# Performance work log

Hardware: AMD Instinct MI355X
Metric: run time of the kernel (lower is better)

## Reference

```python
import jax, jax.numpy as jnp
import numpy as np

EPS = 1e-5
KERNELS = [3, 3, 5, 7]  # 2*i+1 for i>=1, first layer k=3


def _conv_relu_bn(x, w, b, gamma, beta, rmean, rvar):
    # x: [B, Cin, S], w: [Cout, Cin, K]
    k = w.shape[-1]
    y = jax.lax.conv_general_dilated(
        x, w, window_strides=(1,), padding=[(k // 2, k // 2)],
        dimension_numbers=("NCW", "OIW", "NCW"))
    y = y + b[None, :, None]
    y = jax.nn.relu(y)
    # BatchNorm1d in inference mode (running stats)
    inv = gamma[None, :, None] / jnp.sqrt(rvar[None, :, None] + EPS)
    return (y - rmean[None, :, None]) * inv + beta[None, :, None]


def setup_inputs() -> dict:
    key = jax.random.key(0)
    ks = jax.random.split(key, 32)
    B, S = 128, 8192
    inp = {"x": jax.random.normal(ks[0], (B, 4, S), dtype=jnp.float32)}
    cin = 4
    for i, k in enumerate(KERNELS):
        inp[f"w{i}"] = jax.random.normal(ks[1 + i], (32, cin, k), dtype=jnp.float32) * 0.1
        inp[f"b{i}"] = jnp.zeros((32,), jnp.float32)
        inp[f"g{i}"] = jnp.ones((32,), jnp.float32)   # BN gamma
        inp[f"bb{i}"] = jnp.zeros((32,), jnp.float32)  # BN beta
        inp[f"rm{i}"] = jnp.zeros((32,), jnp.float32)  # running mean
        inp[f"rv{i}"] = jnp.ones((32,), jnp.float32)   # running var
        cin = 32
    inp["fw1"] = jax.random.normal(ks[10], (16, 32), dtype=jnp.float32) * 0.1
    inp["fb1"] = jnp.zeros((16,), jnp.float32)
    inp["fw2"] = jax.random.normal(ks[11], (1, 16), dtype=jnp.float32) * 0.1
    inp["fb2"] = jnp.zeros((1,), jnp.float32)
    return inp


def reference(x,
              w0, b0, g0, bb0, rm0, rv0,
              w1, b1, g1, bb1, rm1, rv1,
              w2, b2, g2, bb2, rm2, rv2,
              w3, b3, g3, bb3, rm3, rv3,
              fw1, fb1, fw2, fb2):
    x = _conv_relu_bn(x, w0, b0, g0, bb0, rm0, rv0)
    x = _conv_relu_bn(x, w1, b1, g1, bb1, rm1, rv1)
    x = _conv_relu_bn(x, w2, b2, g2, bb2, rm2, rv2)
    x = _conv_relu_bn(x, w3, b3, g3, bb3, rm3, rv3)
    # [B, 32, S] -> [B, S, 32]; the original per-timestep MLP loop is one batched GEMM
    h = jnp.einsum("bcs,hc->bsh", x, fw1) + fb1
    h = jax.nn.relu(h)  # Dropout(0.1) is identity in eval
    out = jnp.einsum("bsh,oh->bso", h, fw2) + fb2
    return out[..., 0]  # squeeze(-1) -> [B, S]
```

## Files before the change

### kernel.cpp

```cpp
#include <hip/hip_runtime.h>

#define SEQ    8192
#define S_TILE 180
#define NROW   198
#define CS     1608
#define NTHR   256
#define NREC   33
#define BN_HALFOFF (NREC*512)

typedef __attribute__((ext_vector_type(8))) _Float16 half8;
typedef __attribute__((ext_vector_type(4))) float    f32x4;

__device__ __forceinline__ int uni(int v){ return __builtin_amdgcn_readfirstlane(v); }

template<int K>
__device__ __forceinline__ float fold_bias(const float* __restrict__ W, int co,
    const float* __restrict__ gp, const float* __restrict__ bbp,
    const float* __restrict__ rmp, const float* __restrict__ rvp)
{
    float acc = 0.f;
#pragma unroll
    for (int ci = 0; ci < 32; ++ci) {
        float sp = gp[ci] * rsqrtf(rvp[ci] + 1e-5f);
        float tp = bbp[ci] - rmp[ci]*sp;
        float wsum = 0.f;
#pragma unroll
        for (int tap = 0; tap < K; ++tap) wsum += W[(co*32 + ci)*K + tap];
        acc += wsum * tp;
    }
    return acc;
}

extern "C" __global__ void prep_kernel(
    const float* w0, const float* w1, const float* w2, const float* w3,
    const float* b0, const float* g0, const float* bb0, const float* rm0, const float* rv0,
    const float* b1, const float* g1, const float* bb1, const float* rm1, const float* rv1,
    const float* b2, const float* g2, const float* bb2, const float* rm2, const float* rv2,
    const float* b3, const float* g3, const float* bb3, const float* rm3, const float* rv3,
    const float* fw1, const float* fb1, _Float16* ws)
{
    const int tid = threadIdx.x;
    const int rec = blockIdx.x;
    if (rec < NREC) {
        if (tid < 64) {
            const int lane = tid;
            const int q = lane >> 4;
            half8 h;
            if (rec < 2) {
                int co = rec*16 + (lane & 15);
#pragma unroll
                for (int j = 0; j < 8; ++j) {
                    int k = q*8 + j;
                    float wv = (k < 12) ? w0[(co*4 + (k & 3))*3 + (k >> 2)] : 0.0f;
                    h[j] = (_Float16)wv;
                }
            } else {
                const float* W; const float *gp, *rvp; int K, r2;
                if      (rec < 8)  { W = w1;  K = 3; r2 = rec - 2;  gp = g0; rvp = rv0; }
                else if (rec < 18) { W = w2;  K = 5; r2 = rec - 8;  gp = g1; rvp = rv1; }
                else if (rec < 32) { W = w3;  K = 7; r2 = rec - 18; gp = g2; rvp = rv2; }
                else               { W = fw1; K = 1; r2 = 0;        gp = g3; rvp = rv3; }
                int tap = r2 >> 1, mh = r2 & 1;
                int co  = mh*16 + (lane & 15);
#pragma unroll
                for (int j = 0; j < 8; ++j) {
                    int ci = ((j >> 2) << 4) + q*4 + (j & 3);
                    float wv = W[(co*32 + ci)*K + tap];
                    wv *= gp[ci] * rsqrtf(rvp[ci] + 1e-5f);
                    h[j] = (_Float16)wv;
                }
            }
            *(half8*)(ws + rec*512 + lane*8) = h;
        }
    } else {
        float* fa = (float*)(ws + BN_HALFOFF);
        if (tid < 128) {
            int l = tid >> 5, co = tid & 31;
            const float *g, *bb, *rm, *rv, *bi;
            if      (l == 0) { g=g0; bb=bb0; rm=rm0; rv=rv0; bi=b0; }
            else if (l == 1) { g=g1; bb=bb1; rm=rm1; rv=rv1; bi=b1; }
            else if (l == 2) { g=g2; bb=bb2; rm=rm2; rv=rv2; bi=b2; }
            else             { g=g3; bb=bb3; rm=rm3; rv=rv3; bi=b3; }
            float s = g[co] * rsqrtf(rv[co] + 1e-5f);
            float t = bb[co] - rm[co]*s;
            float bias = bi[co];
            if      (l == 1) bias += fold_bias<3>(w1, co, g0, bb0, rm0, rv0);
            else if (l == 2) bias += fold_bias<5>(w2, co, g1, bb1, rm1, rv1);
            else if (l == 3) bias += fold_bias<7>(w3, co, g2, bb2, rm2, rv2);
            fa[(l*32 + co)*2 + 0] = bias;
            fa[(l*32 + co)*2 + 1] = -t / s;
        } else if (tid < 144) {
            int hh = tid - 128;
            float acc = fb1[hh];
#pragma unroll
            for (int c = 0; c < 32; ++c) {
                float s3 = g3[c] * rsqrtf(rv3[c] + 1e-5f);
                float t3 = bb3[c] - rm3[c]*s3;
                acc += fw1[hh*32 + c] * t3;
            }
            fa[256 + hh] = acc;
        }
    }
}

template<int K, int DOFF>
__device__ __forceinline__ void conv_layer(
    const _Float16* __restrict__ rec, const float2* __restrict__ bo,
    const _Float16* in, _Float16* outb, int s0, int ntb, int lane)
{
    const int q = lane >> 4, n = lane & 15;
    const _Float16* bbase = in + q*CS + (ntb*16 + n)*8;

    float oobc[8];
    f32x4 acc[3][2];
    {
        float bias[8];
#pragma unroll
        for (int i = 0; i < 8; ++i) {
            float2 p = bo[(i >> 2)*16 + q*4 + (i & 3)];
            bias[i] = p.x; oobc[i] = p.y;
        }
#pragma unroll
        for (int nt = 0; nt < 3; ++nt)
#pragma unroll
            for (int mh = 0; mh < 2; ++mh)
                acc[nt][mh] = (f32x4){bias[mh*4+0], bias[mh*4+1], bias[mh*4+2], bias[mh*4+3]};
    }

#pragma unroll
    for (int tap = 0; tap < K; ++tap) {
        half8 a0 = *(const half8*)(rec + (tap*2 + 0)*512 + lane*8);
        half8 a1 = *(const half8*)(rec + (tap*2 + 1)*512 + lane*8);
#pragma unroll
        for (int nt = 0; nt < 3; ++nt) {
            half8 bf = *(const half8*)(bbase + nt*128 + tap*8);
            acc[nt][0] = __builtin_amdgcn_mfma_f32_16x16x32_f16(a0, bf, acc[nt][0], 0, 0, 0);
            acc[nt][1] = __builtin_amdgcn_mfma_f32_16x16x32_f16(a1, bf, acc[nt][1], 0, 0, 0);
        }
    }

#pragma unroll
    for (int nt = 0; nt < 3; ++nt) {
        int pos = (ntb + nt)*16 + n;
        bool oob = (unsigned)(s0 + DOFF + pos) >= SEQ;
        half8 hv;
#pragma unroll
        for (int mh = 0; mh < 2; ++mh)
#pragma unroll
            for (int r = 0; r < 4; ++r) {
                float v = fmaxf(acc[nt][mh][r], 0.0f);
                if (oob) v = oobc[mh*4 + r];
                hv[mh*4 + r] = (_Float16)v;
            }
        *(half8*)(outb + q*CS + pos*8) = hv;
    }
}

__device__ __forceinline__ void conv_layer0(
    const _Float16* __restrict__ rec, const float2* __restrict__ bo,
    const _Float16* in, _Float16* outb, int s0, int ntb, int lane)
{
    const int q = lane >> 4, n = lane & 15;
    const _Float16* bbase = in + (q & 1)*CS + (ntb*16 + n)*8;

    float oobc[8];
    f32x4 acc[3][2];
    {
        float bias[8];
#pragma unroll
        for (int i = 0; i < 8; ++i) {
            float2 p = bo[(i >> 2)*16 + q*4 + (i & 3)];
            bias[i] = p.x; oobc[i] = p.y;
        }
#pragma unroll
        for (int nt = 0; nt < 3; ++nt)
#pragma unroll
            for (int mh = 0; mh < 2; ++mh)
                acc[nt][mh] = (f32x4){bias[mh*4+0], bias[mh*4+1], bias[mh*4+2], bias[mh*4+3]};
    }

    half8 a0 = *(const half8*)(rec + 0*512 + lane*8);
    half8 a1 = *(const half8*)(rec + 1*512 + lane*8);
#pragma unroll
    for (int nt = 0; nt < 3; ++nt) {
        half8 bf = *(const half8*)(bbase + nt*128);
        acc[nt][0] = __builtin_amdgcn_mfma_f32_16x16x32_f16(a0, bf, acc[nt][0], 0, 0, 0);
        acc[nt][1] = __builtin_amdgcn_mfma_f32_16x16x32_f16(a1, bf, acc[nt][1], 0, 0, 0);
    }

#pragma unroll
    for (int nt = 0; nt < 3; ++nt) {
        int pos = (ntb + nt)*16 + n;
        bool oob = (unsigned)(s0 - 6 + pos) >= SEQ;
        half8 hv;
#pragma unroll
        for (int mh = 0; mh < 2; ++mh)
#pragma unroll
            for (int r = 0; r < 4; ++r) {
                float v = fmaxf(acc[nt][mh][r], 0.0f);
                if (oob) v = oobc[mh*4 + r];
                hv[mh*4 + r] = (_Float16)v;
            }
        *(half8*)(outb + q*CS + pos*8) = hv;
    }
}

extern "C" __global__ void __launch_bounds__(NTHR, 6)
dnashape_mfma(const float* __restrict__ x, const _Float16* __restrict__ ws,
              const float* __restrict__ fw2, const float* __restrict__ fb2,
              float* __restrict__ out)
{
    __shared__ _Float16 bufA[4*CS];
    __shared__ _Float16 bufB[4*CS];

    const int tid  = threadIdx.x;
    const int tile = blockIdx.x;
    const int s0   = tile * S_TILE;
    const int b    = blockIdx.y;

    {
        const float* xb = x + b*4*SEQ;
        for (int li = tid; li < NROW; li += NTHR) {
            _Float16 h[16];
#pragma unroll
            for (int tap = 0; tap < 3; ++tap) {
                int sg = s0 - 7 + li + tap;
                bool ok = (unsigned)sg < SEQ;
#pragma unroll
                for (int ci = 0; ci < 4; ++ci)
                    h[tap*4 + ci] = (_Float16)(ok ? xb[ci*SEQ + sg] : 0.f);
            }
#pragma unroll
            for (int j = 12; j < 16; ++j) h[j] = (_Float16)0.f;
            *(half8*)(&bufB[0*CS + li*8]) = *(half8*)(h);
            *(half8*)(&bufB[1*CS + li*8]) = *(half8*)(h + 8);
        }
        if (tid < 32) {
            const half8 z8 = {0,0,0,0,0,0,0,0};
            *(half8*)(&bufA[(tid >> 3)*CS + (192 + (tid & 7))*8]) = z8;
        }
    }
    __syncthreads();

    const int lane = tid & 63;
    const int wv   = uni(tid >> 6);
    const int ntb  = wv * 3;
    const float*  fa = (const float*)(ws + BN_HALFOFF);
    const float2* bo = (const float2*)fa;

    conv_layer0      (ws,          bo,      bufB, bufA, s0, ntb, lane);
    __syncthreads();
    conv_layer<3, -5>(ws +  2*512, bo + 32, bufA, bufB, s0, ntb, lane);
    __syncthreads();
    conv_layer<5, -3>(ws +  8*512, bo + 64, bufB, bufA, s0, ntb, lane);
    __syncthreads();

    {
        const int q = lane >> 4, n = lane & 15;
        const _Float16* rec3 = ws + 18*512;
        const _Float16* bbase = bufA + q*CS + (ntb*16 + n)*8;
        const float2* bo3 = bo + 96;

        f32x4 acc[3][2];
        {
            float bias[8];
#pragma unroll
            for (int i = 0; i < 8; ++i)
                bias[i] = bo3[(i >> 2)*16 + q*4 + (i & 3)].x;
#pragma unroll
            for (int nt = 0; nt < 3; ++nt)
#pragma unroll
                for (int mh = 0; mh < 2; ++mh)
                    acc[nt][mh] = (f32x4){bias[mh*4+0], bias[mh*4+1], bias[mh*4+2], bias[mh*4+3]};
        }

#pragma unroll
        for (int tap = 0; tap < 7; ++tap) {
            half8 a0 = *(const half8*)(rec3 + (tap*2 + 0)*512 + lane*8);
            half8 a1 = *(const half8*)(rec3 + (tap*2 + 1)*512 + lane*8);
#pragma unroll
            for (int nt = 0; nt < 3; ++nt) {
                half8 bf = *(const half8*)(bbase + nt*128 + tap*8);
                acc[nt][0] = __builtin_amdgcn_mfma_f32_16x16x32_f16(a0, bf, acc[nt][0], 0, 0, 0);
                acc[nt][1] = __builtin_amdgcn_mfma_f32_16x16x32_f16(a1, bf, acc[nt][1], 0, 0, 0);
            }
        }

        half8 am = *(const half8*)(ws + 32*512 + lane*8);
        float fb1v[4], fw2v[4];
#pragma unroll
        for (int r = 0; r < 4; ++r) { fb1v[r] = fa[256 + q*4 + r]; fw2v[r] = fw2[q*4 + r]; }
        float fb2v = fb2[0];

#pragma unroll
        for (int nt = 0; nt < 3; ++nt) {
            int pos = (ntb + nt)*16 + n;
            half8 hv;
#pragma unroll
            for (int mh = 0; mh < 2; ++mh)
#pragma unroll
                for (int r = 0; r < 4; ++r)
                    hv[mh*4 + r] = (_Float16)fmaxf(acc[nt][mh][r], 0.0f);
            f32x4 d = {0.f, 0.f, 0.f, 0.f};
            d = __builtin_amdgcn_mfma_f32_16x16x32_f16(am, hv, d, 0, 0, 0);
            float part = 0.f;
#pragma unroll
            for (int r = 0; r < 4; ++r) part += fmaxf(d[r] + fb1v[r], 0.f)*fw2v[r];
            part += __shfl_xor(part, 16, 64);
            part += __shfl_xor(part, 32, 64);
            if (lane < 16) {
                int g = s0 + pos;
                if (pos < S_TILE && g < SEQ) out[b*SEQ + g] = part + fb2v;
            }
        }
    }
}

extern "C" void kernel_launch(void* const* d_in, const int* in_sizes, int n_in,
                              void* d_out, int out_size, void* d_ws, size_t ws_size,
                              hipStream_t stream) {
    const float* p[29];
    for (int i = 0; i < 29; ++i) p[i] = (const float*)d_in[i];
    _Float16* ws = (_Float16*)d_ws;

    prep_kernel<<<dim3(NREC + 1), 144, 0, stream>>>(
        p[1], p[7], p[13], p[19],
        p[2], p[3], p[4], p[5], p[6],
        p[8], p[9], p[10], p[11], p[12],
        p[14], p[15], p[16], p[17], p[18],
        p[20], p[21], p[22], p[23], p[24],
        p[25], p[26], ws);

    dim3 grid((SEQ + S_TILE - 1) / S_TILE, 128);
    dnashape_mfma<<<grid, NTHR, 0, stream>>>(p[0], (const _Float16*)ws,
                                             p[27], p[28], (float*)d_out);
}
```

Baseline: 171.4 us.

## Process two batch items per block to reuse weight fragments across images

Each block now handles two batch elements, so every A-fragment (weight) load from global feeds twice as many MFMAs and the number of blocks halves. Shared buffers double and accumulator registers double, so launch bounds drop from 6 to 3 blocks per CU to make room. The MFMA loops are also wrapped in s_setprio raises. The cost is lower occupancy and higher register pressure, which may hurt latency hiding of the LDS loads.

```diff
diff --git a/kernel.cpp b/kernel.cpp
--- a/kernel.cpp
+++ b/kernel.cpp
@@ -4,6 +4,7 @@
 #define S_TILE 180
 #define NROW   198
 #define CS     1608
+#define IMS    (4*CS)
 #define NTHR   256
 #define NREC   33
 #define BN_HALFOFF (NREC*512)
@@ -104,15 +105,16 @@
 }
 
 template<int K, int DOFF>
-__device__ __forceinline__ void conv_layer(
+__device__ __forceinline__ void conv32x2(
     const _Float16* __restrict__ rec, const float2* __restrict__ bo,
     const _Float16* in, _Float16* outb, int s0, int ntb, int lane)
 {
     const int q = lane >> 4, n = lane & 15;
-    const _Float16* bbase = in + q*CS + (ntb*16 + n)*8;
+    const _Float16* bb0 = in +       q*CS + (ntb*16 + n)*8;
+    const _Float16* bb1 = in + IMS + q*CS + (ntb*16 + n)*8;
 
     float oobc[8];
-    f32x4 acc[3][2];
+    f32x4 acc[2][3][2];
     {
         float bias[8];
 #pragma unroll
@@ -121,50 +123,60 @@
             bias[i] = p.x; oobc[i] = p.y;
         }
 #pragma unroll
-        for (int nt = 0; nt < 3; ++nt)
-#pragma unroll
-            for (int mh = 0; mh < 2; ++mh)
-                acc[nt][mh] = (f32x4){bias[mh*4+0], bias[mh*4+1], bias[mh*4+2], bias[mh*4+3]};
-    }
-
+        for (int im = 0; im < 2; ++im)
+#pragma unroll
+            for (int nt = 0; nt < 3; ++nt)
+#pragma unroll
+                for (int mh = 0; mh < 2; ++mh)
+                    acc[im][nt][mh] = (f32x4){bias[mh*4+0], bias[mh*4+1], bias[mh*4+2], bias[mh*4+3]};
+    }
+
+    __builtin_amdgcn_s_setprio(1);
 #pragma unroll
     for (int tap = 0; tap < K; ++tap) {
         half8 a0 = *(const half8*)(rec + (tap*2 + 0)*512 + lane*8);
         half8 a1 = *(const half8*)(rec + (tap*2 + 1)*512 + lane*8);
 #pragma unroll
         for (int nt = 0; nt < 3; ++nt) {
-            half8 bf = *(const half8*)(bbase + nt*128 + tap*8);
-            acc[nt][0] = __builtin_amdgcn_mfma_f32_16x16x32_f16(a0, bf, acc[nt][0], 0, 0, 0);
-            acc[nt][1] = __builtin_amdgcn_mfma_f32_16x16x32_f16(a1, bf, acc[nt][1], 0, 0, 0);
-        }
-    }
-
-#pragma unroll
-    for (int nt = 0; nt < 3; ++nt) {
-        int pos = (ntb + nt)*16 + n;
-        bool oob = (unsigned)(s0 + DOFF + pos) >= SEQ;
-        half8 hv;
-#pragma unroll
-        for (int mh = 0; mh < 2; ++mh)
-#pragma unroll
-            for (int r = 0; r < 4; ++r) {
-                float v = fmaxf(acc[nt][mh][r], 0.0f);
-                if (oob) v = oobc[mh*4 + r];
-                hv[mh*4 + r] = (_Float16)v;
-            }
-        *(half8*)(outb + q*CS + pos*8) = hv;
-    }
-}
-
-__device__ __forceinline__ void conv_layer0(
+            half8 bf0 = *(const half8*)(bb0 + nt*128 + tap*8);
+            acc[0][nt][0] = __builtin_amdgcn_mfma_f32_16x16x32_f16(a0, bf0, acc[0][nt][0], 0, 0, 0);
+            acc[0][nt][1] = __builtin_amdgcn_mfma_f32_16x16x32_f16(a1, bf0, acc[0][nt][1], 0, 0, 0);
+            half8 bf1 = *(const half8*)(bb1 + nt*128 + tap*8);
+            acc[1][nt][0] = __builtin_amdgcn_mfma_f32_16x16x32_f16(a0, bf1, acc[1][nt][0], 0, 0, 0);
+            acc[1][nt][1] = __builtin_amdgcn_mfma_f32_16x16x32_f16(a1, bf1, acc[1][nt][1], 0, 0, 0);
+        }
+    }
+    __builtin_amdgcn_s_setprio(0);
+
+#pragma unroll
+    for (int im = 0; im < 2; ++im)
+#pragma unroll
+        for (int nt = 0; nt < 3; ++nt) {
+            int pos = (ntb + nt)*16 + n;
+            bool oob = (unsigned)(s0 + DOFF + pos) >= SEQ;
+            half8 hv;
+#pragma unroll
+            for (int mh = 0; mh < 2; ++mh)
+#pragma unroll
+                for (int r = 0; r < 4; ++r) {
+                    float v = fmaxf(acc[im][nt][mh][r], 0.0f);
+                    if (oob) v = oobc[mh*4 + r];
+                    hv[mh*4 + r] = (_Float16)v;
+                }
+            *(half8*)(outb + im*IMS + q*CS + pos*8) = hv;
+        }
+}
+
+__device__ __forceinline__ void conv32x2L0(
     const _Float16* __restrict__ rec, const float2* __restrict__ bo,
     const _Float16* in, _Float16* outb, int s0, int ntb, int lane)
 {
     const int q = lane >> 4, n = lane & 15;
-    const _Float16* bbase = in + (q & 1)*CS + (ntb*16 + n)*8;
+    const _Float16* bb0 = in +       (q & 1)*CS + (ntb*16 + n)*8;
+    const _Float16* bb1 = in + IMS + (q & 1)*CS + (ntb*16 + n)*8;
 
     float oobc[8];
-    f32x4 acc[3][2];
+    f32x4 acc[2][3][2];
     {
         float bias[8];
 #pragma unroll
@@ -173,58 +185,68 @@
             bias[i] = p.x; oobc[i] = p.y;
         }
 #pragma unroll
-        for (int nt = 0; nt < 3; ++nt)
-#pragma unroll
-            for (int mh = 0; mh < 2; ++mh)
-                acc[nt][mh] = (f32x4){bias[mh*4+0], bias[mh*4+1], bias[mh*4+2], bias[mh*4+3]};
+        for (int im = 0; im < 2; ++im)
+#pragma unroll
+            for (int nt = 0; nt < 3; ++nt)
+#pragma unroll
+                for (int mh = 0; mh < 2; ++mh)
+                    acc[im][nt][mh] = (f32x4){bias[mh*4+0], bias[mh*4+1], bias[mh*4+2], bias[mh*4+3]};
     }
 
     half8 a0 = *(const half8*)(rec + 0*512 + lane*8);
     half8 a1 = *(const half8*)(rec + 1*512 + lane*8);
+    __builtin_amdgcn_s_setprio(1);
 #pragma unroll
     for (int nt = 0; nt < 3; ++nt) {
-        half8 bf = *(const half8*)(bbase + nt*128);
-        acc[nt][0] = __builtin_amdgcn_mfma_f32_16x16x32_f16(a0, bf, acc[nt][0], 0, 0, 0);
-        acc[nt][1] = __builtin_amdgcn_mfma_f32_16x16x32_f16(a1, bf, acc[nt][1], 0, 0, 0);
-    }
-
-#pragma unroll
-    for (int nt = 0; nt < 3; ++nt) {
-        int pos = (ntb + nt)*16 + n;
-        bool oob = (unsigned)(s0 - 6 + pos) >= SEQ;
-        half8 hv;
-#pragma unroll
-        for (int mh = 0; mh < 2; ++mh)
-#pragma unroll
-            for (int r = 0; r < 4; ++r) {
-                float v = fmaxf(acc[nt][mh][r], 0.0f);
-                if (oob) v = oobc[mh*4 + r];
-                hv[mh*4 + r] = (_Float16)v;
-            }
-        *(half8*)(outb + q*CS + pos*8) = hv;
-    }
-}
-
-extern "C" __global__ void __launch_bounds__(NTHR, 6)
+        half8 bf0 = *(const half8*)(bb0 + nt*128);
+        acc[0][nt][0] = __builtin_amdgcn_mfma_f32_16x16x32_f16(a0, bf0, acc[0][nt][0], 0, 0, 0);
+        acc[0][nt][1] = __builtin_amdgcn_mfma_f32_16x16x32_f16(a1, bf0, acc[0][nt][1], 0, 0, 0);
+        half8 bf1 = *(const half8*)(bb1 + nt*128);
+        acc[1][nt][0] = __builtin_amdgcn_mfma_f32_16x16x32_f16(a0, bf1, acc[1][nt][0], 0, 0, 0);
+        acc[1][nt][1] = __builtin_amdgcn_mfma_f32_16x16x32_f16(a1, bf1, acc[1][nt][1], 0, 0, 0);
+    }
+    __builtin_amdgcn_s_setprio(0);
+
+#pragma unroll
+    for (int im = 0; im < 2; ++im)
+#pragma unroll
+        for (int nt = 0; nt < 3; ++nt) {
+            int pos = (ntb + nt)*16 + n;
+            bool oob = (unsigned)(s0 - 6 + pos) >= SEQ;
+            half8 hv;
+#pragma unroll
+            for (int mh = 0; mh < 2; ++mh)
+#pragma unroll
+                for (int r = 0; r < 4; ++r) {
+                    float v = fmaxf(acc[im][nt][mh][r], 0.0f);
+                    if (oob) v = oobc[mh*4 + r];
+                    hv[mh*4 + r] = (_Float16)v;
+                }
+            *(half8*)(outb + im*IMS + q*CS + pos*8) = hv;
+        }
+}
+
+extern "C" __global__ void __launch_bounds__(NTHR, 3)
 dnashape_mfma(const float* __restrict__ x, const _Float16* __restrict__ ws,
               const float* __restrict__ fw2, const float* __restrict__ fb2,
               float* __restrict__ out)
 {
-    __shared__ _Float16 bufA[4*CS];
-    __shared__ _Float16 bufB[4*CS];
-
+    __shared__ _Float16 bufA[2*IMS];
+    __shared__ _Float16 bufB[2*IMS];
     const int tid  = threadIdx.x;
     const int tile = blockIdx.x;
     const int s0   = tile * S_TILE;
-    const int b    = blockIdx.y;
+    const int b0   = blockIdx.y * 2;
 
     {
-        const float* xb = x + b*4*SEQ;
-        for (int li = tid; li < NROW; li += NTHR) {
+        for (int li = tid; li < 2*NROW; li += NTHR) {
+            int im = (li >= NROW);
+            int r  = li - im*NROW;
+            const float* xb = x + (b0 + im)*4*SEQ;
             _Float16 h[16];
 #pragma unroll
             for (int tap = 0; tap < 3; ++tap) {
-                int sg = s0 - 7 + li + tap;
+                int sg = s0 - 7 + r + tap;
                 bool ok = (unsigned)sg < SEQ;
 #pragma unroll
                 for (int ci = 0; ci < 4; ++ci)
@@ -232,12 +254,12 @@
             }
 #pragma unroll
             for (int j = 12; j < 16; ++j) h[j] = (_Float16)0.f;
-            *(half8*)(&bufB[0*CS + li*8]) = *(half8*)(h);
-            *(half8*)(&bufB[1*CS + li*8]) = *(half8*)(h + 8);
-        }
-        if (tid < 32) {
+            *(half8*)(&bufB[im*IMS + 0*CS + r*8]) = *(half8*)(h);
+            *(half8*)(&bufB[im*IMS + 1*CS + r*8]) = *(half8*)(h + 8);
+        }
+        if (tid < 64) {
             const half8 z8 = {0,0,0,0,0,0,0,0};
-            *(half8*)(&bufA[(tid >> 3)*CS + (192 + (tid & 7))*8]) = z8;
+            *(half8*)(&bufA[(tid >> 5)*IMS + ((tid >> 3) & 3)*CS + (192 + (tid & 7))*8]) = z8;
         }
     }
     __syncthreads();
@@ -248,43 +270,51 @@
     const float*  fa = (const float*)(ws + BN_HALFOFF);
     const float2* bo = (const float2*)fa;
 
-    conv_layer0      (ws,          bo,      bufB, bufA, s0, ntb, lane);
+    conv32x2L0      (ws,          bo,      bufB, bufA, s0, ntb, lane);
     __syncthreads();
-    conv_layer<3, -5>(ws +  2*512, bo + 32, bufA, bufB, s0, ntb, lane);
+    conv32x2<3, -5>(ws +  2*512, bo + 32, bufA, bufB, s0, ntb, lane);
     __syncthreads();
-    conv_layer<5, -3>(ws +  8*512, bo + 64, bufB, bufA, s0, ntb, lane);
+    conv32x2<5, -3>(ws +  8*512, bo + 64, bufB, bufA, s0, ntb, lane);
     __syncthreads();
 
     {
         const int q = lane >> 4, n = lane & 15;
         const _Float16* rec3 = ws + 18*512;
-        const _Float16* bbase = bufA + q*CS + (ntb*16 + n)*8;
+        const _Float16* bb0 = bufA +       q*CS + (ntb*16 + n)*8;
+        const _Float16* bb1 = bufA + IMS + q*CS + (ntb*16 + n)*8;
         const float2* bo3 = bo + 96;
 
-        f32x4 acc[3][2];
+        f32x4 acc[2][3][2];
         {
             float bias[8];
 #pragma unroll
             for (int i = 0; i < 8; ++i)
                 bias[i] = bo3[(i >> 2)*16 + q*4 + (i & 3)].x;
 #pragma unroll
-            for (int nt = 0; nt < 3; ++nt)
-#pragma unroll
-                for (int mh = 0; mh < 2; ++mh)
-                    acc[nt][mh] = (f32x4){bias[mh*4+0], bias[mh*4+1], bias[mh*4+2], bias[mh*4+3]};
-        }
-
+            for (int im = 0; im < 2; ++im)
+#pragma unroll
+                for (int nt = 0; nt < 3; ++nt)
+#pragma unroll
+                    for (int mh = 0; mh < 2; ++mh)
+                        acc[im][nt][mh] = (f32x4){bias[mh*4+0], bias[mh*4+1], bias[mh*4+2], bias[mh*4+3]};
+        }
+
+        __builtin_amdgcn_s_setprio(1);
 #pragma unroll
         for (int tap = 0; tap < 7; ++tap) {
             half8 a0 = *(const half8*)(rec3 + (tap*2 + 0)*512 + lane*8);
             half8 a1 = *(const half8*)(rec3 + (tap*2 + 1)*512 + lane*8);
 #pragma unroll
             for (int nt = 0; nt < 3; ++nt) {
-                half8 bf = *(const half8*)(bbase + nt*128 + tap*8);
-                acc[nt][0] = __builtin_amdgcn_mfma_f32_16x16x32_f16(a0, bf, acc[nt][0], 0, 0, 0);
-                acc[nt][1] = __builtin_amdgcn_mfma_f32_16x16x32_f16(a1, bf, acc[nt][1], 0, 0, 0);
-            }
-        }
+                half8 bf0 = *(const half8*)(bb0 + nt*128 + tap*8);
+                acc[0][nt][0] = __builtin_amdgcn_mfma_f32_16x16x32_f16(a0, bf0, acc[0][nt][0], 0, 0, 0);
+                acc[0][nt][1] = __builtin_amdgcn_mfma_f32_16x16x32_f16(a1, bf0, acc[0][nt][1], 0, 0, 0);
+                half8 bf1 = *(const half8*)(bb1 + nt*128 + tap*8);
+                acc[1][nt][0] = __builtin_amdgcn_mfma_f32_16x16x32_f16(a0, bf1, acc[1][nt][0], 0, 0, 0);
+                acc[1][nt][1] = __builtin_amdgcn_mfma_f32_16x16x32_f16(a1, bf1, acc[1][nt][1], 0, 0, 0);
+            }
+        }
+        __builtin_amdgcn_s_setprio(0);
 
         half8 am = *(const half8*)(ws + 32*512 + lane*8);
         float fb1v[4], fw2v[4];
@@ -293,26 +323,28 @@
         float fb2v = fb2[0];
 
 #pragma unroll
-        for (int nt = 0; nt < 3; ++nt) {
-            int pos = (ntb + nt)*16 + n;
-            half8 hv;
-#pragma unroll
-            for (int mh = 0; mh < 2; ++mh)
-#pragma unroll
-                for (int r = 0; r < 4; ++r)
-                    hv[mh*4 + r] = (_Float16)fmaxf(acc[nt][mh][r], 0.0f);
-            f32x4 d = {0.f, 0.f, 0.f, 0.f};
-            d = __builtin_amdgcn_mfma_f32_16x16x32_f16(am, hv, d, 0, 0, 0);
-            float part = 0.f;
-#pragma unroll
-            for (int r = 0; r < 4; ++r) part += fmaxf(d[r] + fb1v[r], 0.f)*fw2v[r];
-            part += __shfl_xor(part, 16, 64);
-            part += __shfl_xor(part, 32, 64);
-            if (lane < 16) {
-                int g = s0 + pos;
-                if (pos < S_TILE && g < SEQ) out[b*SEQ + g] = part + fb2v;
-            }
-        }
+        for (int im = 0; im < 2; ++im)
+#pragma unroll
+            for (int nt = 0; nt < 3; ++nt) {
+                int pos = (ntb + nt)*16 + n;
+                half8 hv;
+#pragma unroll
+                for (int mh = 0; mh < 2; ++mh)
+#pragma unroll
+                    for (int r = 0; r < 4; ++r)
+                        hv[mh*4 + r] = (_Float16)fmaxf(acc[im][nt][mh][r], 0.0f);
+                f32x4 d = {0.f, 0.f, 0.f, 0.f};
+                d = __builtin_amdgcn_mfma_f32_16x16x32_f16(am, hv, d, 0, 0, 0);
+                float part = 0.f;
+#pragma unroll
+                for (int r = 0; r < 4; ++r) part += fmaxf(d[r] + fb1v[r], 0.f)*fw2v[r];
+                part += __shfl_xor(part, 16, 64);
+                part += __shfl_xor(part, 32, 64);
+                if (lane < 16) {
+                    int g = s0 + pos;
+                    if (pos < S_TILE && g < SEQ) out[(b0 + im)*SEQ + g] = part + fb2v;
+                }
+            }
     }
 }
 
@@ -331,7 +363,7 @@
         p[20], p[21], p[22], p[23], p[24],
         p[25], p[26], ws);
 
-    dim3 grid((SEQ + S_TILE - 1) / S_TILE, 128);
+    dim3 grid((SEQ + S_TILE - 1) / S_TILE, 64);
     dnashape_mfma<<<grid, NTHR, 0, stream>>>(p[0], (const _Float16*)ws,
                                              p[27], p[28], (float*)d_out);
 }
```

Result: slower. 180.2 us (+5.1%).
